# Kernel tuning notes

Hardware: AMD Instinct MI355X
Metric: run time of the kernel (lower is better)

The kernel has to match this reference:

```python
import jax, jax.numpy as jnp
import numpy as np

K = 7
TOP_M = 2
TOP_U = 2
TAU = 1.2
EPS = 1e-9
LN_EPS = 1e-5


def setup_inputs() -> dict:
    key = jax.random.key(0)
    ks = jax.random.split(key, 8)
    B, T, D, R = 4, 2048, 1024, 128
    return {
        "h": jax.random.normal(ks[0], (B, T, D), jnp.float32),
        "gate_w": jax.random.normal(ks[1], (K, D), jnp.float32) * (1.0 / np.sqrt(D)),
        "gate_b": jnp.zeros((K,), jnp.float32),
        "U_w": jax.random.normal(ks[2], (R, D), jnp.float32) * (1.0 / np.sqrt(D)),
        "V": jax.random.normal(ks[3], (K, R, D), jnp.float32) / np.sqrt(R),
        "ln_g": jnp.ones((D,), jnp.float32),
        "ln_b": jnp.zeros((D,), jnp.float32),
        "comp_w": jax.random.normal(ks[4], (D, D), jnp.float32) * (1.0 / np.sqrt(D)),
        "comp_b": jnp.zeros((D,), jnp.float32),
    }


def _layernorm(x, g, b):
    mu = x.mean(-1, keepdims=True)
    var = ((x - mu) ** 2).mean(-1, keepdims=True)
    return (x - mu) * jax.lax.rsqrt(var + LN_EPS) * g + b


def reference(h, gate_w, gate_b, U_w, V, ln_g, ln_b, comp_w, comp_b):
    # gates: [B,T,K]
    G = jax.nn.softmax(jnp.einsum('btd,kd->btk', h, gate_w) + gate_b, axis=-1)
    # top-m selected facets
    _, seli = jax.lax.top_k(G, TOP_M)                      # [B,T,m]
    sel_mask = jax.nn.one_hot(seli, K, dtype=jnp.float32).sum(-2) > 0
    unselected = jnp.where(sel_mask, 0.0, G)
    # top-u among unselected (TOP_U < K - TOP_M here)
    _, ui = jax.lax.top_k(unselected, TOP_U)
    u_mask = jax.nn.one_hot(ui, K, dtype=jnp.float32).sum(-2) > 0
    unselected = jnp.where(u_mask, unselected, 0.0)
    leftover = unselected / jnp.maximum(unselected.sum(-1, keepdims=True), EPS)
    leftover = jax.nn.softmax(jnp.log(jnp.maximum(leftover, EPS)) / TAU, axis=-1)
    # factorized per-facet states: [B,T,K,D]
    basis = jnp.einsum('btd,rd->btr', h, U_w)
    states = jnp.einsum('btr,krd->btkd', basis, V)
    states = _layernorm(states, ln_g, ln_b)
    # mix leftover facets, compress, pool='last'
    b = jnp.einsum('btk,btkd->btd', leftover, states)
    b = jnp.einsum('btd,ed->bte', b, comp_w) + comp_b
    b = b[:, -1, :]
    return (b, G)
```

## Files before the change

### kernel.cpp

```cpp
#include <hip/hip_runtime.h>
#include <math.h>

#define KEXP 7
#define DDIM 1024
#define RDIM 128
#define TSEQ 2048
#define BBATCH 4
#define TAU_C 1.2f
#define EPS_C 1e-9f
#define LN_EPS_C 1e-5f

#define WS_S     0
#define WS_BASIS 28672
#define WS_W     (WS_BASIS + 512)
#define WS_PSTAT (WS_W + 32)

__device__ __forceinline__ float dot4(float4 a, float4 b) {
    return fmaf(a.x, b.x, fmaf(a.y, b.y, fmaf(a.z, b.z, a.w * b.w)));
}


__device__ __forceinline__ void role_basis(int idx, const float* __restrict__ h,
                                           const float* __restrict__ U_w,
                                           float* __restrict__ ws, int lane, int wv) {
    const int b = idx >> 3;
    const int chunk = idx & 7;
    const float4* h4 = (const float4*)(h + ((size_t)b * TSEQ + (TSEQ - 1)) * DDIM);
    float4 hf[4];
#pragma unroll
    for (int j = 0; j < 4; ++j) hf[j] = h4[j * 64 + lane];
    const int r0 = chunk * 16 + wv * 4;
    float part[4];
#pragma unroll
    for (int rr = 0; rr < 4; ++rr) {
        const float4* u4 = (const float4*)(U_w + (size_t)(r0 + rr) * DDIM);
        float a = 0.f;
#pragma unroll
        for (int j = 0; j < 4; ++j) a += dot4(hf[j], u4[j * 64 + lane]);
        part[rr] = a;
    }
#pragma unroll
    for (int off = 32; off > 0; off >>= 1)
#pragma unroll
        for (int rr = 0; rr < 4; ++rr)
            part[rr] += __shfl_xor(part[rr], off, 64);
    if (lane == 0) {
#pragma unroll
        for (int rr = 0; rr < 4; ++rr)
            ws[WS_BASIS + b * RDIM + r0 + rr] = part[rr];
    }
}

__device__ __forceinline__ void role_weights(int b, const float* __restrict__ h,
                                             const float* __restrict__ gate_w,
                                             const float* __restrict__ gate_b,
                                             float* __restrict__ ws, float* sA,
                                             int tid, int lane, int wv) {
    const float4* h4 = (const float4*)(h + ((size_t)b * TSEQ + (TSEQ - 1)) * DDIM);
    for (int e = wv; e < KEXP; e += 4) {
        const float4* gw4 = (const float4*)(gate_w + (size_t)e * DDIM);
        float a = 0.f;
#pragma unroll
        for (int j = 0; j < 4; ++j) a += dot4(h4[j * 64 + lane], gw4[j * 64 + lane]);
#pragma unroll
        for (int off = 32; off > 0; off >>= 1) a += __shfl_xor(a, off, 64);
        if (lane == 0) sA[e] = a + gate_b[e];
    }
    __syncthreads();
    if (tid == 0) {
        float l0[KEXP], m0 = -1e30f;
#pragma unroll
        for (int j = 0; j < KEXP; ++j) { l0[j] = sA[j]; m0 = fmaxf(m0, l0[j]); }
        float es0 = 0.f, g[KEXP];
#pragma unroll
        for (int j = 0; j < KEXP; ++j) { g[j] = expf(l0[j] - m0); es0 += g[j]; }
        const float inv0 = 1.f / es0;
#pragma unroll
        for (int j = 0; j < KEXP; ++j) g[j] *= inv0;
        int i1 = 0;
        for (int j = 1; j < KEXP; ++j) if (g[j] > g[i1]) i1 = j;
        int i2 = -1;
        for (int j = 0; j < KEXP; ++j)
            if (j != i1 && (i2 < 0 || g[j] > g[i2])) i2 = j;
        int i3 = -1;
        for (int j = 0; j < KEXP; ++j)
            if (j != i1 && j != i2 && (i3 < 0 || g[j] > g[i3])) i3 = j;
        int i4 = -1;
        for (int j = 0; j < KEXP; ++j)
            if (j != i1 && j != i2 && j != i3 && (i4 < 0 || g[j] > g[i4])) i4 = j;
        float s = fmaxf(g[i3] + g[i4], EPS_C);
        float p[KEXP];
#pragma unroll
        for (int j = 0; j < KEXP; ++j) p[j] = 0.f;
        p[i3] = g[i3] / s;
        p[i4] = g[i4] / s;
        float l[KEXP], m = -1e30f;
#pragma unroll
        for (int j = 0; j < KEXP; ++j) {
            l[j] = logf(fmaxf(p[j], EPS_C)) * (1.f / TAU_C);
            m = fmaxf(m, l[j]);
        }
        float es = 0.f, w[KEXP];
#pragma unroll
        for (int j = 0; j < KEXP; ++j) { w[j] = expf(l[j] - m); es += w[j]; }
        const float inv = 1.f / es;
        float wsum = 0.f;
#pragma unroll
        for (int j = 0; j < KEXP; ++j) { w[j] *= inv; wsum += w[j]; ws[WS_W + b * 8 + j] = w[j]; }
        ws[WS_W + b * 8 + 7] = wsum;
    }
}

__device__ __forceinline__ void gate_chunk(int c, const float* __restrict__ h,
                                           const float* __restrict__ gate_w,
                                           const float* __restrict__ gate_b,
                                           float* __restrict__ G,
                                           int lane, int wv) {
    const float4* gw4 = (const float4*)gate_w;
    float4 gw[KEXP][4];
#pragma unroll
    for (int k = 0; k < KEXP; ++k)
#pragma unroll
        for (int j = 0; j < 4; ++j)
            gw[k][j] = gw4[k * 256 + j * 64 + lane];
    float gb[KEXP];
#pragma unroll
    for (int k = 0; k < KEXP; ++k) gb[k] = gate_b[k];

    const int row0 = c * 16 + wv * 4;
#pragma unroll
    for (int r = 0; r < 4; ++r) {
        const int row = row0 + r;
        const float4* h4 = (const float4*)(h + (size_t)row * DDIM);
        float acc[KEXP];
#pragma unroll
        for (int k = 0; k < KEXP; ++k) acc[k] = 0.f;
#pragma unroll
        for (int j = 0; j < 4; ++j) {
            float4 hv = h4[j * 64 + lane];
#pragma unroll
            for (int k = 0; k < KEXP; ++k) {
                acc[k] = fmaf(hv.x, gw[k][j].x, acc[k]);
                acc[k] = fmaf(hv.y, gw[k][j].y, acc[k]);
                acc[k] = fmaf(hv.z, gw[k][j].z, acc[k]);
                acc[k] = fmaf(hv.w, gw[k][j].w, acc[k]);
            }
        }
#pragma unroll
        for (int k = 0; k < KEXP; ++k) {
#pragma unroll
            for (int off = 32; off > 0; off >>= 1)
                acc[k] += __shfl_xor(acc[k], off, 64);
        }
        float m = -1e30f;
#pragma unroll
        for (int k = 0; k < KEXP; ++k) { acc[k] += gb[k]; m = fmaxf(m, acc[k]); }
        float e[KEXP];
        float s = 0.f;
#pragma unroll
        for (int k = 0; k < KEXP; ++k) { e[k] = expf(acc[k] - m); s += e[k]; }
        const float inv = 1.f / s;
        if (lane == 0) {
#pragma unroll
            for (int k = 0; k < KEXP; ++k) G[row * KEXP + k] = e[k] * inv;
        }
    }
}

__device__ __forceinline__ void role_sv(int idx, const float* __restrict__ V,
                                        float* __restrict__ ws, float* sA, float4* sB,
                                        int tid) {
    const int k = idx >> 4;
    const int chunk = idx & 15;
    const int col = tid & 15;
    const int rc = tid >> 4;

    sA[tid] = ws[WS_BASIS + tid];
    sA[tid + 256] = ws[WS_BASIS + tid + 256];
    __syncthreads();

    const float4* V4 = (const float4*)(V + (size_t)k * RDIM * DDIM);
    float4 acc[BBATCH];
#pragma unroll
    for (int b = 0; b < BBATCH; ++b) acc[b] = make_float4(0.f, 0.f, 0.f, 0.f);
#pragma unroll
    for (int rr = 0; rr < 8; ++rr) {
        const int r = rc * 8 + rr;
        float4 v = V4[(size_t)r * 256 + chunk * 16 + col];
#pragma unroll
        for (int b = 0; b < BBATCH; ++b) {
            const float br = sA[b * RDIM + r];
            acc[b].x = fmaf(br, v.x, acc[b].x);
            acc[b].y = fmaf(br, v.y, acc[b].y);
            acc[b].z = fmaf(br, v.z, acc[b].z);
            acc[b].w = fmaf(br, v.w, acc[b].w);
        }
    }
#pragma unroll
    for (int b = 0; b < BBATCH; ++b) sB[(rc * 4 + b) * 16 + col] = acc[b];
    __syncthreads();

    if (tid < 64) {
        const int b = tid >> 4;
        const int c = tid & 15;
        float4 s4 = make_float4(0.f, 0.f, 0.f, 0.f);
#pragma unroll
        for (int q = 0; q < 16; ++q) {
            float4 p = sB[(q * 4 + b) * 16 + c];
            s4.x += p.x; s4.y += p.y; s4.z += p.z; s4.w += p.w;
        }
        ((float4*)(ws + WS_S))[(size_t)(b * KEXP + k) * 256 + chunk * 16 + c] = s4;
        float p1 = s4.x + s4.y + s4.z + s4.w;
        float p2 = dot4(s4, s4);
#pragma unroll
        for (int off = 8; off > 0; off >>= 1) {
            p1 += __shfl_xor(p1, off, 64);
            p2 += __shfl_xor(p2, off, 64);
        }
        if (c == 0) {
            ws[WS_PSTAT + ((b * KEXP + k) * 16 + chunk) * 2 + 0] = p1;
            ws[WS_PSTAT + ((b * KEXP + k) * 16 + chunk) * 2 + 1] = p2;
        }
    }
}

__device__ __forceinline__ void role_comp(int cb_idx, const float* __restrict__ ws,
                                          const float* __restrict__ ln_g,
                                          const float* __restrict__ ln_b,
                                          const float* __restrict__ comp_w,
                                          const float* __restrict__ comp_b,
                                          float* __restrict__ out,
                                          float* sA, float4* sB,
                                          int tid, int lane, int wv) {
    if (tid < BBATCH * KEXP) {
        const int b = tid / KEXP;
        const int k = tid % KEXP;
        float s1 = 0.f, s2 = 0.f;
#pragma unroll
        for (int c = 0; c < 16; ++c) {
            s1 += ws[WS_PSTAT + ((b * KEXP + k) * 16 + c) * 2 + 0];
            s2 += ws[WS_PSTAT + ((b * KEXP + k) * 16 + c) * 2 + 1];
        }
        const float mu = s1 * (1.f / (float)DDIM);
        const float var = s2 * (1.f / (float)DDIM) - mu * mu;
        const float rs = rsqrtf(var + LN_EPS_C);
        const float w = ws[WS_W + b * 8 + k];
        sA[b * KEXP + k] = w * rs;
        sA[28 + b * KEXP + k] = w * rs * mu;
    }
    __syncthreads();
    if (tid < BBATCH) {
        float c = 0.f;
#pragma unroll
        for (int k = 0; k < KEXP; ++k) c += sA[28 + tid * KEXP + k];
        sA[56 + tid] = c;
        sA[60 + tid] = ws[WS_W + tid * 8 + 7];
    }
    __syncthreads();

    {
        const float4 g4 = ((const float4*)ln_g)[tid];
        const float4 b4 = ((const float4*)ln_b)[tid];
        const float4* s4p = (const float4*)(ws + WS_S);
#pragma unroll
        for (int b = 0; b < BBATCH; ++b) {
            float4 s = make_float4(0.f, 0.f, 0.f, 0.f);
#pragma unroll
            for (int k = 0; k < KEXP; ++k) {
                const float a = sA[b * KEXP + k];
                float4 v = s4p[(size_t)(b * KEXP + k) * 256 + tid];
                s.x = fmaf(a, v.x, s.x);
                s.y = fmaf(a, v.y, s.y);
                s.z = fmaf(a, v.z, s.z);
                s.w = fmaf(a, v.w, s.w);
            }
            const float C = sA[56 + b], wsum = sA[60 + b];
            float4 o;
            o.x = g4.x * (s.x - C) + b4.x * wsum;
            o.y = g4.y * (s.y - C) + b4.y * wsum;
            o.z = g4.z * (s.z - C) + b4.z * wsum;
            o.w = g4.w * (s.w - C) + b4.w * wsum;
            sB[b * 256 + tid] = o;
        }
    }
    __syncthreads();

    const int e = cb_idx * 4 + wv;
    const float4* cw4 = (const float4*)(comp_w + (size_t)e * DDIM);
    float acc[BBATCH] = {0.f, 0.f, 0.f, 0.f};
#pragma unroll
    for (int j = 0; j < 4; ++j) {
        float4 c = cw4[j * 64 + lane];
#pragma unroll
        for (int b = 0; b < BBATCH; ++b) acc[b] += dot4(c, sB[b * 256 + j * 64 + lane]);
    }
#pragma unroll
    for (int b = 0; b < BBATCH; ++b)
#pragma unroll
        for (int off = 32; off > 0; off >>= 1)
            acc[b] += __shfl_xor(acc[b], off, 64);
    if (lane == 0) {
        const float cb = comp_b[e];
#pragma unroll
        for (int b = 0; b < BBATCH; ++b)
            out[b * DDIM + e] = acc[b] + cb;
    }
}

__global__ __launch_bounds__(256) void k_prep(const float* __restrict__ h,
                                              const float* __restrict__ gate_w,
                                              const float* __restrict__ gate_b,
                                              const float* __restrict__ U_w,
                                              float* __restrict__ ws) {
    __shared__ float sA[8];
    const int tid = threadIdx.x;
    const int lane = tid & 63;
    const int wv = tid >> 6;
    if (blockIdx.x < 32) role_basis(blockIdx.x, h, U_w, ws, lane, wv);
    else                 role_weights(blockIdx.x - 32, h, gate_w, gate_b, ws, sA, tid, lane, wv);
}

__global__ __launch_bounds__(256) void k_main(const float* __restrict__ h,
                                              const float* __restrict__ gate_w,
                                              const float* __restrict__ gate_b,
                                              const float* __restrict__ V,
                                              float* __restrict__ G,
                                              float* __restrict__ ws) {
    __shared__ float sA[512];
    __shared__ float4 sB[1024];
    const int bid = blockIdx.x;
    const int tid = threadIdx.x;
    const int lane = tid & 63;
    const int wv = tid >> 6;
    if (bid < 112) role_sv(bid, V, ws, sA, sB, tid);
    else           gate_chunk(bid - 112, h, gate_w, gate_b, G, lane, wv);
}

__global__ __launch_bounds__(256) void k_comp2(const float* __restrict__ ws,
                                               const float* __restrict__ ln_g,
                                               const float* __restrict__ ln_b,
                                               const float* __restrict__ comp_w,
                                               const float* __restrict__ comp_b,
                                               float* __restrict__ out) {
    __shared__ float sA[512];
    __shared__ float4 sB[1024];
    const int tid = threadIdx.x;
    const int lane = tid & 63;
    const int wv = tid >> 6;
    role_comp(blockIdx.x, ws, ln_g, ln_b, comp_w, comp_b, out, sA, sB, tid, lane, wv);
}

extern "C" void kernel_launch(void* const* d_in, const int* in_sizes, int n_in,
                              void* d_out, int out_size, void* d_ws, size_t ws_size,
                              hipStream_t stream) {
    const float* h      = (const float*)d_in[0];
    const float* gate_w = (const float*)d_in[1];
    const float* gate_b = (const float*)d_in[2];
    const float* U_w    = (const float*)d_in[3];
    const float* V      = (const float*)d_in[4];
    const float* ln_g   = (const float*)d_in[5];
    const float* ln_b   = (const float*)d_in[6];
    const float* comp_w = (const float*)d_in[7];
    const float* comp_b = (const float*)d_in[8];

    float* out = (float*)d_out;
    float* G   = out + BBATCH * DDIM;
    float* ws  = (float*)d_ws;

    k_prep<<<36, 256, 0, stream>>>(h, gate_w, gate_b, U_w, ws);
    k_main<<<624, 256, 0, stream>>>(h, gate_w, gate_b, V, G, ws);
    k_comp2<<<256, 256, 0, stream>>>(ws, ln_g, ln_b, comp_w, comp_b, out);
}
```

Baseline: 25.80 us.

## Fuse prep stage into consumers, cutting three kernel launches to two

Removes the separate prep kernel. Each of the 112 SV blocks now recomputes the full 4x128 basis projection (h_last · U_w) redundantly in shared memory before its V slice. The gate-softmax and leftover-weight computation moves into the compression blocks of a second kernel, which also runs the full-sequence gate chunks. This drops one launch and its dependency barrier, but every SV block now rereads all of U_w (512 KB), and each comp block redoes the weight computation.

Measured after the change: 35.45 us. +37.4%, slower.

```diff
diff --git a/kernel.cpp b/kernel.cpp
--- a/kernel.cpp
+++ b/kernel.cpp
@@ -11,104 +11,44 @@
 #define LN_EPS_C 1e-5f
 
 #define WS_S     0
-#define WS_BASIS 28672
-#define WS_W     (WS_BASIS + 512)
-#define WS_PSTAT (WS_W + 32)
+#define WS_PSTAT 28672
 
 __device__ __forceinline__ float dot4(float4 a, float4 b) {
     return fmaf(a.x, b.x, fmaf(a.y, b.y, fmaf(a.z, b.z, a.w * b.w)));
 }
 
-
-__device__ __forceinline__ void role_basis(int idx, const float* __restrict__ h,
-                                           const float* __restrict__ U_w,
-                                           float* __restrict__ ws, int lane, int wv) {
-    const int b = idx >> 3;
-    const int chunk = idx & 7;
-    const float4* h4 = (const float4*)(h + ((size_t)b * TSEQ + (TSEQ - 1)) * DDIM);
-    float4 hf[4];
-#pragma unroll
-    for (int j = 0; j < 4; ++j) hf[j] = h4[j * 64 + lane];
-    const int r0 = chunk * 16 + wv * 4;
-    float part[4];
-#pragma unroll
-    for (int rr = 0; rr < 4; ++rr) {
-        const float4* u4 = (const float4*)(U_w + (size_t)(r0 + rr) * DDIM);
-        float a = 0.f;
-#pragma unroll
-        for (int j = 0; j < 4; ++j) a += dot4(hf[j], u4[j * 64 + lane]);
-        part[rr] = a;
-    }
-#pragma unroll
-    for (int off = 32; off > 0; off >>= 1)
-#pragma unroll
-        for (int rr = 0; rr < 4; ++rr)
-            part[rr] += __shfl_xor(part[rr], off, 64);
-    if (lane == 0) {
-#pragma unroll
-        for (int rr = 0; rr < 4; ++rr)
-            ws[WS_BASIS + b * RDIM + r0 + rr] = part[rr];
-    }
-}
-
-__device__ __forceinline__ void role_weights(int b, const float* __restrict__ h,
-                                             const float* __restrict__ gate_w,
-                                             const float* __restrict__ gate_b,
-                                             float* __restrict__ ws, float* sA,
-                                             int tid, int lane, int wv) {
-    const float4* h4 = (const float4*)(h + ((size_t)b * TSEQ + (TSEQ - 1)) * DDIM);
-    for (int e = wv; e < KEXP; e += 4) {
-        const float4* gw4 = (const float4*)(gate_w + (size_t)e * DDIM);
-        float a = 0.f;
-#pragma unroll
-        for (int j = 0; j < 4; ++j) a += dot4(h4[j * 64 + lane], gw4[j * 64 + lane]);
-#pragma unroll
-        for (int off = 32; off > 0; off >>= 1) a += __shfl_xor(a, off, 64);
-        if (lane == 0) sA[e] = a + gate_b[e];
-    }
-    __syncthreads();
-    if (tid == 0) {
-        float l0[KEXP], m0 = -1e30f;
-#pragma unroll
-        for (int j = 0; j < KEXP; ++j) { l0[j] = sA[j]; m0 = fmaxf(m0, l0[j]); }
-        float es0 = 0.f, g[KEXP];
-#pragma unroll
-        for (int j = 0; j < KEXP; ++j) { g[j] = expf(l0[j] - m0); es0 += g[j]; }
-        const float inv0 = 1.f / es0;
-#pragma unroll
-        for (int j = 0; j < KEXP; ++j) g[j] *= inv0;
-        int i1 = 0;
-        for (int j = 1; j < KEXP; ++j) if (g[j] > g[i1]) i1 = j;
-        int i2 = -1;
-        for (int j = 0; j < KEXP; ++j)
-            if (j != i1 && (i2 < 0 || g[j] > g[i2])) i2 = j;
-        int i3 = -1;
-        for (int j = 0; j < KEXP; ++j)
-            if (j != i1 && j != i2 && (i3 < 0 || g[j] > g[i3])) i3 = j;
-        int i4 = -1;
-        for (int j = 0; j < KEXP; ++j)
-            if (j != i1 && j != i2 && j != i3 && (i4 < 0 || g[j] > g[i4])) i4 = j;
-        float s = fmaxf(g[i3] + g[i4], EPS_C);
-        float p[KEXP];
-#pragma unroll
-        for (int j = 0; j < KEXP; ++j) p[j] = 0.f;
-        p[i3] = g[i3] / s;
-        p[i4] = g[i4] / s;
-        float l[KEXP], m = -1e30f;
-#pragma unroll
-        for (int j = 0; j < KEXP; ++j) {
-            l[j] = logf(fmaxf(p[j], EPS_C)) * (1.f / TAU_C);
-            m = fmaxf(m, l[j]);
-        }
-        float es = 0.f, w[KEXP];
-#pragma unroll
-        for (int j = 0; j < KEXP; ++j) { w[j] = expf(l[j] - m); es += w[j]; }
-        const float inv = 1.f / es;
-        float wsum = 0.f;
-#pragma unroll
-        for (int j = 0; j < KEXP; ++j) { w[j] *= inv; wsum += w[j]; ws[WS_W + b * 8 + j] = w[j]; }
-        ws[WS_W + b * 8 + 7] = wsum;
-    }
+__device__ __forceinline__ void leftover_from_probs(const float* g, float* wout) {
+    int i1 = 0;
+    for (int j = 1; j < KEXP; ++j) if (g[j] > g[i1]) i1 = j;
+    int i2 = -1;
+    for (int j = 0; j < KEXP; ++j)
+        if (j != i1 && (i2 < 0 || g[j] > g[i2])) i2 = j;
+    int i3 = -1;
+    for (int j = 0; j < KEXP; ++j)
+        if (j != i1 && j != i2 && (i3 < 0 || g[j] > g[i3])) i3 = j;
+    int i4 = -1;
+    for (int j = 0; j < KEXP; ++j)
+        if (j != i1 && j != i2 && j != i3 && (i4 < 0 || g[j] > g[i4])) i4 = j;
+    float s = fmaxf(g[i3] + g[i4], EPS_C);
+    float p[KEXP];
+#pragma unroll
+    for (int j = 0; j < KEXP; ++j) p[j] = 0.f;
+    p[i3] = g[i3] / s;
+    p[i4] = g[i4] / s;
+    float l[KEXP], m = -1e30f;
+#pragma unroll
+    for (int j = 0; j < KEXP; ++j) {
+        l[j] = logf(fmaxf(p[j], EPS_C)) * (1.f / TAU_C);
+        m = fmaxf(m, l[j]);
+    }
+    float es = 0.f, w[KEXP];
+#pragma unroll
+    for (int j = 0; j < KEXP; ++j) { w[j] = expf(l[j] - m); es += w[j]; }
+    const float inv = 1.f / es;
+    float wsum = 0.f;
+#pragma unroll
+    for (int j = 0; j < KEXP; ++j) { w[j] *= inv; wsum += w[j]; wout[j] = w[j]; }
+    wout[7] = wsum;
 }
 
 __device__ __forceinline__ void gate_chunk(int c, const float* __restrict__ h,
@@ -167,37 +107,87 @@
     }
 }
 
-__device__ __forceinline__ void role_sv(int idx, const float* __restrict__ V,
-                                        float* __restrict__ ws, float* sA, float4* sB,
-                                        int tid) {
-    const int k = idx >> 4;
-    const int chunk = idx & 15;
-    const int col = tid & 15;
-    const int rc = tid >> 4;
-
-    sA[tid] = ws[WS_BASIS + tid];
-    sA[tid + 256] = ws[WS_BASIS + tid + 256];
-    __syncthreads();
-
-    const float4* V4 = (const float4*)(V + (size_t)k * RDIM * DDIM);
-    float4 acc[BBATCH];
-#pragma unroll
-    for (int b = 0; b < BBATCH; ++b) acc[b] = make_float4(0.f, 0.f, 0.f, 0.f);
-#pragma unroll
-    for (int rr = 0; rr < 8; ++rr) {
-        const int r = rc * 8 + rr;
-        float4 v = V4[(size_t)r * 256 + chunk * 16 + col];
+__global__ __launch_bounds__(256) void k_sv2(const float* __restrict__ h,
+                                             const float* __restrict__ U_w,
+                                             const float* __restrict__ V,
+                                             float* __restrict__ ws) {
+    const int k = blockIdx.x >> 4;
+    const int chunk = blockIdx.x & 15;
+    const int tid = threadIdx.x;
+    const int lane = tid & 63;
+    const int wv = tid >> 6;
+
+    __shared__ float basis_sh[BBATCH * RDIM];
+    __shared__ float4 part[16 * BBATCH * 16];
+
+    {
+        float4 hf[BBATCH][4];
 #pragma unroll
         for (int b = 0; b < BBATCH; ++b) {
-            const float br = sA[b * RDIM + r];
-            acc[b].x = fmaf(br, v.x, acc[b].x);
-            acc[b].y = fmaf(br, v.y, acc[b].y);
-            acc[b].z = fmaf(br, v.z, acc[b].z);
-            acc[b].w = fmaf(br, v.w, acc[b].w);
-        }
-    }
-#pragma unroll
-    for (int b = 0; b < BBATCH; ++b) sB[(rc * 4 + b) * 16 + col] = acc[b];
+            const float4* h4 = (const float4*)(h + ((size_t)b * TSEQ + (TSEQ - 1)) * DDIM);
+#pragma unroll
+            for (int j = 0; j < 4; ++j) hf[b][j] = h4[j * 64 + lane];
+        }
+        const int rbase = wv * 32;
+        for (int rr0 = 0; rr0 < 32; rr0 += 2) {
+            float4 u0[4], u1[4];
+            const float4* ua = (const float4*)(U_w + (size_t)(rbase + rr0) * DDIM);
+            const float4* ub = (const float4*)(U_w + (size_t)(rbase + rr0 + 1) * DDIM);
+#pragma unroll
+            for (int j = 0; j < 4; ++j) { u0[j] = ua[j * 64 + lane]; u1[j] = ub[j * 64 + lane]; }
+            float p0[BBATCH], p1[BBATCH];
+#pragma unroll
+            for (int b = 0; b < BBATCH; ++b) { p0[b] = 0.f; p1[b] = 0.f; }
+#pragma unroll
+            for (int j = 0; j < 4; ++j) {
+#pragma unroll
+                for (int b = 0; b < BBATCH; ++b) {
+                    p0[b] += dot4(hf[b][j], u0[j]);
+                    p1[b] += dot4(hf[b][j], u1[j]);
+                }
+            }
+#pragma unroll
+            for (int off = 32; off > 0; off >>= 1) {
+#pragma unroll
+                for (int b = 0; b < BBATCH; ++b) {
+                    p0[b] += __shfl_xor(p0[b], off, 64);
+                    p1[b] += __shfl_xor(p1[b], off, 64);
+                }
+            }
+            if (lane == 0) {
+#pragma unroll
+                for (int b = 0; b < BBATCH; ++b) {
+                    basis_sh[b * RDIM + rbase + rr0] = p0[b];
+                    basis_sh[b * RDIM + rbase + rr0 + 1] = p1[b];
+                }
+            }
+        }
+    }
+    __syncthreads();
+
+    {
+        const int col = tid & 15;
+        const int rc = tid >> 4;
+        const float4* V4 = (const float4*)(V + (size_t)k * RDIM * DDIM);
+        float4 acc[BBATCH];
+#pragma unroll
+        for (int b = 0; b < BBATCH; ++b) acc[b] = make_float4(0.f, 0.f, 0.f, 0.f);
+#pragma unroll
+        for (int rr = 0; rr < 8; ++rr) {
+            const int r = rc * 8 + rr;
+            float4 v = V4[(size_t)r * 256 + chunk * 16 + col];
+#pragma unroll
+            for (int b = 0; b < BBATCH; ++b) {
+                const float br = basis_sh[b * RDIM + r];
+                acc[b].x = fmaf(br, v.x, acc[b].x);
+                acc[b].y = fmaf(br, v.y, acc[b].y);
+                acc[b].z = fmaf(br, v.z, acc[b].z);
+                acc[b].w = fmaf(br, v.w, acc[b].w);
+            }
+        }
+#pragma unroll
+        for (int b = 0; b < BBATCH; ++b) part[(rc * 4 + b) * 16 + col] = acc[b];
+    }
     __syncthreads();
 
     if (tid < 64) {
@@ -206,7 +196,7 @@
         float4 s4 = make_float4(0.f, 0.f, 0.f, 0.f);
 #pragma unroll
         for (int q = 0; q < 16; ++q) {
-            float4 p = sB[(q * 4 + b) * 16 + c];
+            float4 p = part[(q * 4 + b) * 16 + c];
             s4.x += p.x; s4.y += p.y; s4.z += p.z; s4.w += p.w;
         }
         ((float4*)(ws + WS_S))[(size_t)(b * KEXP + k) * 256 + chunk * 16 + c] = s4;
@@ -224,14 +214,65 @@
     }
 }
 
-__device__ __forceinline__ void role_comp(int cb_idx, const float* __restrict__ ws,
-                                          const float* __restrict__ ln_g,
-                                          const float* __restrict__ ln_b,
-                                          const float* __restrict__ comp_w,
-                                          const float* __restrict__ comp_b,
-                                          float* __restrict__ out,
-                                          float* sA, float4* sB,
-                                          int tid, int lane, int wv) {
+__global__ __launch_bounds__(256) void k_gc(const float* __restrict__ h,
+                                            const float* __restrict__ gate_w,
+                                            const float* __restrict__ gate_b,
+                                            const float* __restrict__ ws,
+                                            const float* __restrict__ ln_g,
+                                            const float* __restrict__ ln_b,
+                                            const float* __restrict__ comp_w,
+                                            const float* __restrict__ comp_b,
+                                            float* __restrict__ G,
+                                            float* __restrict__ out) {
+    const int bid = blockIdx.x;
+    const int tid = threadIdx.x;
+    const int lane = tid & 63;
+    const int wv = tid >> 6;
+
+    __shared__ float sA[64];
+    __shared__ float wsh[BBATCH][8];
+    __shared__ float4 sB[BBATCH * 256];
+
+    if (bid < 512) {
+        gate_chunk(bid, h, gate_w, gate_b, G, lane, wv);
+        return;
+    }
+
+    {
+        const int b = wv;
+        const float4* h4 = (const float4*)(h + ((size_t)b * TSEQ + (TSEQ - 1)) * DDIM);
+        const float4* gw4 = (const float4*)gate_w;
+        float acc[KEXP];
+#pragma unroll
+        for (int k = 0; k < KEXP; ++k) acc[k] = 0.f;
+#pragma unroll
+        for (int j = 0; j < 4; ++j) {
+            float4 hv = h4[j * 64 + lane];
+#pragma unroll
+            for (int k = 0; k < KEXP; ++k)
+                acc[k] += dot4(hv, gw4[k * 256 + j * 64 + lane]);
+        }
+#pragma unroll
+        for (int k = 0; k < KEXP; ++k) {
+#pragma unroll
+            for (int off = 32; off > 0; off >>= 1)
+                acc[k] += __shfl_xor(acc[k], off, 64);
+        }
+        if (lane == 0) {
+            float g[KEXP], m = -1e30f;
+#pragma unroll
+            for (int k = 0; k < KEXP; ++k) { g[k] = acc[k] + gate_b[k]; m = fmaxf(m, g[k]); }
+            float es = 0.f;
+#pragma unroll
+            for (int k = 0; k < KEXP; ++k) { g[k] = expf(g[k] - m); es += g[k]; }
+            const float inv = 1.f / es;
+#pragma unroll
+            for (int k = 0; k < KEXP; ++k) g[k] *= inv;
+            leftover_from_probs(g, &wsh[b][0]);
+        }
+    }
+    __syncthreads();
+
     if (tid < BBATCH * KEXP) {
         const int b = tid / KEXP;
         const int k = tid % KEXP;
@@ -244,7 +285,7 @@
         const float mu = s1 * (1.f / (float)DDIM);
         const float var = s2 * (1.f / (float)DDIM) - mu * mu;
         const float rs = rsqrtf(var + LN_EPS_C);
-        const float w = ws[WS_W + b * 8 + k];
+        const float w = wsh[b][k];
         sA[b * KEXP + k] = w * rs;
         sA[28 + b * KEXP + k] = w * rs * mu;
     }
@@ -254,7 +295,7 @@
 #pragma unroll
         for (int k = 0; k < KEXP; ++k) c += sA[28 + tid * KEXP + k];
         sA[56 + tid] = c;
-        sA[60 + tid] = ws[WS_W + tid * 8 + 7];
+        sA[60 + tid] = wsh[tid][7];
     }
     __syncthreads();
 
@@ -285,7 +326,7 @@
     }
     __syncthreads();
 
-    const int e = cb_idx * 4 + wv;
+    const int e = (bid - 512) * 4 + wv;
     const float4* cw4 = (const float4*)(comp_w + (size_t)e * DDIM);
     float acc[BBATCH] = {0.f, 0.f, 0.f, 0.f};
 #pragma unroll
@@ -305,49 +346,6 @@
         for (int b = 0; b < BBATCH; ++b)
             out[b * DDIM + e] = acc[b] + cb;
     }
-}
-
-__global__ __launch_bounds__(256) void k_prep(const float* __restrict__ h,
-                                              const float* __restrict__ gate_w,
-                                              const float* __restrict__ gate_b,
-                                              const float* __restrict__ U_w,
-                                              float* __restrict__ ws) {
-    __shared__ float sA[8];
-    const int tid = threadIdx.x;
-    const int lane = tid & 63;
-    const int wv = tid >> 6;
-    if (blockIdx.x < 32) role_basis(blockIdx.x, h, U_w, ws, lane, wv);
-    else                 role_weights(blockIdx.x - 32, h, gate_w, gate_b, ws, sA, tid, lane, wv);
-}
-
-__global__ __launch_bounds__(256) void k_main(const float* __restrict__ h,
-                                              const float* __restrict__ gate_w,
-                                              const float* __restrict__ gate_b,
-                                              const float* __restrict__ V,
-                                              float* __restrict__ G,
-                                              float* __restrict__ ws) {
-    __shared__ float sA[512];
-    __shared__ float4 sB[1024];
-    const int bid = blockIdx.x;
-    const int tid = threadIdx.x;
-    const int lane = tid & 63;
-    const int wv = tid >> 6;
-    if (bid < 112) role_sv(bid, V, ws, sA, sB, tid);
-    else           gate_chunk(bid - 112, h, gate_w, gate_b, G, lane, wv);
-}
-
-__global__ __launch_bounds__(256) void k_comp2(const float* __restrict__ ws,
-                                               const float* __restrict__ ln_g,
-                                               const float* __restrict__ ln_b,
-                                               const float* __restrict__ comp_w,
-                                               const float* __restrict__ comp_b,
-                                               float* __restrict__ out) {
-    __shared__ float sA[512];
-    __shared__ float4 sB[1024];
-    const int tid = threadIdx.x;
-    const int lane = tid & 63;
-    const int wv = tid >> 6;
-    role_comp(blockIdx.x, ws, ln_g, ln_b, comp_w, comp_b, out, sA, sB, tid, lane, wv);
 }
 
 extern "C" void kernel_launch(void* const* d_in, const int* in_sizes, int n_in,
@@ -367,7 +365,7 @@
     float* G   = out + BBATCH * DDIM;
     float* ws  = (float*)d_ws;
 
-    k_prep<<<36, 256, 0, stream>>>(h, gate_w, gate_b, U_w, ws);
-    k_main<<<624, 256, 0, stream>>>(h, gate_w, gate_b, V, G, ws);
-    k_comp2<<<256, 256, 0, stream>>>(ws, ln_g, ln_b, comp_w, comp_b, out);
-}
+    k_sv2<<<KEXP * 16, 256, 0, stream>>>(h, U_w, V, ws);
+    k_gc<<<768, 256, 0, stream>>>(h, gate_w, gate_b, ws, ln_g, ln_b,
+                                  comp_w, comp_b, G, out);
+}
```
